# Kernel tuning notes

Measured on AMD Instinct MI355X. Metric: run time of the kernel, lower is better.

The kernel has to match this reference:

```python
import jax, jax.numpy as jnp
import numpy as np

ROPE_BASE = 10000.0

def _rope(x, positions):
    # x: (B, h, T, d); standard half-split rotary embedding with d_key = d
    d = x.shape[-1]
    inv_freq = 1.0 / (ROPE_BASE ** (jnp.arange(0, d // 2, dtype=jnp.float32) / (d // 2)))
    ang = positions.astype(jnp.float32)[:, None] * inv_freq[None, :]  # (T, d/2)
    cos, sin = jnp.cos(ang), jnp.sin(ang)
    x1, x2 = x[..., : d // 2], x[..., d // 2 :]
    return jnp.concatenate([x1 * cos - x2 * sin, x1 * sin + x2 * cos], axis=-1)


def setup_inputs() -> dict:
    key = jax.random.key(0)
    k1, k2, k3 = jax.random.split(key, 3)
    B, T, d, h = 2, 2048, 768, 8
    std = d ** -0.5
    x = jax.random.normal(k1, (B, T, d), dtype=jnp.float32)
    M = jax.random.normal(k2, (d, h * d), dtype=jnp.float32) * std
    V = jax.random.normal(k3, (d, h * d), dtype=jnp.float32) * std
    positions = jnp.arange(T, dtype=jnp.int32)
    return {"x": x, "M": M, "V": V, "positions": positions}


def reference(x, M, V, positions):
    B, T, d = x.shape
    h = M.shape[1] // d
    scale = 1.0 / jnp.sqrt(jnp.float32(d))
    # Q = RoPE(X @ M), K = RoPE(X) broadcast across heads, val = X @ V
    Q = (x @ M).reshape(B, T, h, d).transpose(0, 2, 1, 3)   # (B,h,T,d)
    val = (x @ V).reshape(B, T, h, d).transpose(0, 2, 1, 3)  # (B,h,T,d)
    K = jnp.broadcast_to(x[:, None, :, :], (B, h, T, d))     # (B,h,T,d)
    Q = _rope(Q, positions)
    K = _rope(K, positions)
    scores = jnp.einsum("bhqd,bhkd->bhqk", Q, K) * scale     # (B,h,T,T)
    causal = jnp.tril(jnp.ones((T, T), dtype=bool))          # True = keep
    scores = jnp.where(causal[None, None], scores, -jnp.inf)
    attn = jax.nn.softmax(scores, axis=-1)
    out = jnp.einsum("bhqk,bhkd->bhqd", attn, val)
    return out.sum(axis=1)  # sum over heads -> (B,T,d)
```

## Files before the change

kernel.cpp:

```cpp
#include <hip/hip_runtime.h>
#include <hip/hip_bf16.h>

typedef __bf16 bf16x8 __attribute__((ext_vector_type(8)));
typedef float f32x4 __attribute__((ext_vector_type(4)));
typedef float f32x16 __attribute__((ext_vector_type(16)));

#define SCALE 0.03608439182435161f
#define NEGINF (-1e30f)

static __device__ __forceinline__ ushort f2bf(float f) {
    union { float f; unsigned u; } v; v.f = f;
    unsigned r = (v.u + 0x7fff + ((v.u >> 16) & 1)) >> 16;
    return (ushort)r;
}
static __device__ __forceinline__ float bf2f(ushort u) {
    union { unsigned u; float f; } v; v.u = ((unsigned)u) << 16;
    return v.f;
}

static __device__ __forceinline__ void gload16(const void* g, void* lds) {
    __builtin_amdgcn_global_load_lds((const __attribute__((address_space(1))) void*)g,
                                     (__attribute__((address_space(3))) void*)lds, 16, 0, 0);
}

#define PHASEB do { asm volatile("s_waitcnt vmcnt(0) lgkmcnt(0)" ::: "memory"); \
                    __builtin_amdgcn_s_barrier(); \
                    asm volatile("" ::: "memory"); } while (0)
#define BARL do { asm volatile("s_waitcnt lgkmcnt(0)" ::: "memory"); \
                  __builtin_amdgcn_s_barrier(); \
                  asm volatile("" ::: "memory"); } while (0)

__global__ void k_convx(const float* __restrict__ x, ushort* __restrict__ xb, int n4) {
    int i = blockIdx.x * blockDim.x + threadIdx.x;
    if (i >= n4) return;
    float4 v = ((const float4*)x)[i];
    ushort4 o; o.x = f2bf(v.x); o.y = f2bf(v.y); o.z = f2bf(v.z); o.w = f2bf(v.w);
    ((ushort4*)xb)[i] = o;
}

__global__ void k_tconv(const float* __restrict__ in, ushort* __restrict__ out, int R, int C) {
    __shared__ float ts[32][33];
    int r0 = blockIdx.x * 32, c0 = blockIdx.y * 32;
    int lr = threadIdx.x >> 5, lc = threadIdx.x & 31;
#pragma unroll
    for (int i = 0; i < 4; i++) ts[lr + i * 8][lc] = in[(r0 + lr + i * 8) * C + c0 + lc];
    __syncthreads();
#pragma unroll
    for (int i = 0; i < 4; i++) out[(c0 + lr + i * 8) * R + r0 + lc] = f2bf(ts[lc][lr + i * 8]);
}

template <int EPI>
__global__ __launch_bounds__(256) void k_gemm(const ushort* __restrict__ A,
                                              const ushort* __restrict__ Bt,
                                              ushort* __restrict__ out) {
    __shared__ ushort As[128 * 32];
    __shared__ ushort Bs[128 * 32];
    const int m0 = blockIdx.x * 128, n0 = blockIdx.y * 128;
    const int tid = threadIdx.x, lane = tid & 63, wid = tid >> 6;
    const int wm = (wid >> 1) * 64, wn = (wid & 1) * 64;
    const int l15 = lane & 15, l4 = lane >> 4;
    const int srow = tid >> 2, scol = (tid & 3) * 8;
    f32x4 acc[4][4] = {};

    for (int kt = 0; kt < 768; kt += 32) {
        gload16(&A[(size_t)(m0 + srow) * 768 + kt + scol],       (char*)As + wid * 1024);
        gload16(&A[(size_t)(m0 + 64 + srow) * 768 + kt + scol],  (char*)As + 4096 + wid * 1024);
        gload16(&Bt[(size_t)(n0 + srow) * 768 + kt + scol],      (char*)Bs + wid * 1024);
        gload16(&Bt[(size_t)(n0 + 64 + srow) * 768 + kt + scol], (char*)Bs + 4096 + wid * 1024);
        PHASEB;
        bf16x8 af[4], bfr[4];
#pragma unroll
        for (int m = 0; m < 4; m++)
            af[m] = *(const bf16x8*)&As[(wm + m * 16 + l15) * 32 + l4 * 8];
#pragma unroll
        for (int n = 0; n < 4; n++)
            bfr[n] = *(const bf16x8*)&Bs[(wn + n * 16 + l15) * 32 + l4 * 8];
#pragma unroll
        for (int m = 0; m < 4; m++)
#pragma unroll
            for (int n = 0; n < 4; n++)
                acc[m][n] = __builtin_amdgcn_mfma_f32_16x16x32_bf16(af[m], bfr[n], acc[m][n], 0, 0, 0);
        BARL;
    }

#pragma unroll
    for (int m = 0; m < 4; m++) {
#pragma unroll
        for (int n = 0; n < 4; n++) {
#pragma unroll
            for (int r = 0; r < 4; r++) {
                int row = m0 + wm + m * 16 + (lane >> 4) * 4 + r;
                int col = n0 + wn + n * 16 + (lane & 15);
                float v = acc[m][n][r];
                int idx;
                if (EPI == 0) {
                    int b = row >> 11, t = row & 2047;
                    int hh = col / 768, dd = col - hh * 768;
                    idx = ((b * 8 + hh) * 2048 + t) * 768 + dd;
                } else {
                    int hh = row / 768, dd = row - hh * 768;
                    int b = col >> 11, t = col & 2047;
                    idx = ((b * 8 + hh) * 768 + dd) * 2048 + t;
                }
                out[idx] = f2bf(v);
            }
        }
    }
}

__global__ void k_ropek(const float* __restrict__ x, ushort* __restrict__ Kr,
                        const int* __restrict__ pos, int nrows) {
    int i = blockIdx.x * blockDim.x + threadIdx.x;
    int row = i / 96, j4 = (i % 96) * 4;
    if (row >= nrows) return;
    float p = (float)pos[row & 2047];
    float4 x1 = *(const float4*)&x[row * 768 + j4];
    float4 x2 = *(const float4*)&x[row * 768 + 384 + j4];
    ushort4 o1, o2;
    float a1[4] = {x1.x, x1.y, x1.z, x1.w};
    float a2[4] = {x2.x, x2.y, x2.z, x2.w};
#pragma unroll
    for (int k = 0; k < 4; k++) {
        float inv = exp2f(-(float)(j4 + k) * (13.287712379549449f / 384.0f));
        float ang = p * inv;
        float s, c; sincosf(ang, &s, &c);
        ((ushort*)&o1)[k] = f2bf(a1[k] * c - a2[k] * s);
        ((ushort*)&o2)[k] = f2bf(a1[k] * s + a2[k] * c);
    }
    *(ushort4*)&Kr[row * 768 + j4] = o1;
    *(ushort4*)&Kr[row * 768 + 384 + j4] = o2;
}

__global__ __launch_bounds__(512, 2) void k_attn(const ushort* Qr, const ushort* __restrict__ Kr,
                                                 const ushort* __restrict__ valT,
                                                 const int* __restrict__ pos, ushort* Oh) {
    __shared__ alignas(128) char Qs[98304];
    __shared__ alignas(128) char pool[65536];

    const int p = blockIdx.x, hh = blockIdx.y, b = blockIdx.z;
    const int bh = b * 8 + hh;
    const int tid = threadIdx.x, lane = tid & 63, wid = tid >> 6;
    const int g = wid & 3, qh = wid >> 2;
    const int l31 = lane & 31, hi = lane >> 5;
    const int hi16 = hi << 4;

    const int row0 = tid >> 4, col16 = tid & 15;
    const int swz = (col16 << 4) ^ ((row0 & 15) << 4);

    const int arow = g * 32 + l31;
    const int qrow = qh * 32 + l31;
    const int asw = (arow & 15) << 4;
    const int qsw = (qrow & 15) << 4;

    char* Pb = pool + 32768;
    float2* stats = (float2*)(pool + 49152);

    const char* Kb0 = (const char*)Kr + ((size_t)(b * 2048 + row0)) * 1536 + swz;
    const char* Vb0 = (const char*)valT + ((size_t)(bh * 768 + row0)) * 4096 + swz;

    for (int ti = 0; ti < 2; ti++) {
        const int qt = ti ? (31 - p) : p;
        const int q0 = qt * 64;
        const int nkb = (qt + 2) >> 1;
        const int qg = q0 + qrow;

        const char* qsrc = (const char*)Qr + ((size_t)(bh * 2048 + q0 + row0)) * 1536 + swz;
#pragma unroll
        for (int r = 0; r < 12; r++)
            gload16(qsrc + (r >> 1) * 256 + (size_t)(r & 1) * 49152,
                    Qs + (r >> 1) * 16384 + (r & 1) * 8192 + wid * 1024);
#pragma unroll
        for (int r = 0; r < 4; r++)
            gload16(Kb0 + (size_t)r * 49152, pool + r * 8192 + wid * 1024);

        PHASEB;

        {
            const int rr = tid >> 3;
            const int gb0 = (tid & 7) * 16;
            const int rsw = (rr & 15) << 4;
            const float pf = (float)pos[q0 + rr];
#pragma unroll
            for (int c = 0; c < 3; c++) {
#pragma unroll
                for (int h2 = 0; h2 < 2; h2++) {
                    int gb = gb0 + h2 * 128;
                    char* p1 = Qs + c * 16384 + rr * 256 + (gb ^ rsw);
                    char* p2 = Qs + (c + 3) * 16384 + rr * 256 + (gb ^ rsw);
                    uint4 u1 = *(uint4*)p1, u2 = *(uint4*)p2;
                    uint4 o1, o2;
                    ushort* a1 = (ushort*)&u1; ushort* a2 = (ushort*)&u2;
                    ushort* b1 = (ushort*)&o1; ushort* b2 = (ushort*)&o2;
#pragma unroll
                    for (int k = 0; k < 8; k++) {
                        float dv = (float)(c * 128 + (gb >> 1) + k);
                        float inv = exp2f(-dv * (13.287712379549449f / 384.0f));
                        float ang = pf * inv;
                        float sn, cs; __sincosf(ang, &sn, &cs);
                        float x1 = bf2f(a1[k]), x2 = bf2f(a2[k]);
                        b1[k] = f2bf((x1 * cs - x2 * sn) * SCALE);
                        b2[k] = f2bf((x1 * sn + x2 * cs) * SCALE);
                    }
                    *(uint4*)p1 = o1; *(uint4*)p2 = o2;
                }
            }
        }
        BARL;

        float m_r = NEGINF, l_r = 0.f;
        f32x16 oacc[6] = {};

        for (int kb = 0; kb < nkb; kb++) {
            const char* kc = Kb0 + (size_t)kb * 196608;
            const char* vc = Vb0 + (size_t)kb * 256;
            const bool nx = (kb + 1 < nkb);
            const bool nm = (kb * 128 + 127 > q0);

            f32x16 sacc = {};
#pragma unroll
            for (int c = 0; c < 6; c++) {
                PHASEB;
                if (c < 5) {
#pragma unroll
                    for (int r = 0; r < 4; r++)
                        gload16(kc + (c + 1) * 256 + (size_t)r * 49152,
                                pool + ((c + 1) & 1) * 32768 + r * 8192 + wid * 1024);
                } else {
#pragma unroll
                    for (int r = 0; r < 4; r++)
                        gload16(vc + (size_t)r * 131072, pool + r * 8192 + wid * 1024);
                }
                const char* kbuf = pool + (c & 1) * 32768;
                const char* qcb = Qs + c * 16384;
                __builtin_amdgcn_s_setprio(1);
#pragma unroll
                for (int s = 0; s < 8; s++) {
                    bf16x8 a = *(const bf16x8*)(kbuf + arow * 256 + ((s * 32 + hi16) ^ asw));
                    bf16x8 bq = *(const bf16x8*)(qcb + qrow * 256 + ((s * 32 + hi16) ^ qsw));
                    sacc = __builtin_amdgcn_mfma_f32_32x32x16_bf16(a, bq, sacc, 0, 0, 0);
                }
                __builtin_amdgcn_s_setprio(0);
            }

            BARL;

            const int kbase_ = kb * 128 + g * 32 + 4 * hi;
            float mloc = NEGINF, sloc = 0.f;
            if (nm) {
#pragma unroll
                for (int r = 0; r < 16; r++) {
                    int kg = kbase_ + (r & 3) + 8 * (r >> 2);
                    if (kg <= qg) mloc = fmaxf(mloc, sacc[r]);
                }
                mloc = fmaxf(mloc, __shfl_xor(mloc, 32));
#pragma unroll
                for (int r = 0; r < 16; r++) {
                    int kg = kbase_ + (r & 3) + 8 * (r >> 2);
                    sloc += (kg <= qg) ? __expf(sacc[r] - mloc) : 0.f;
                }
            } else {
#pragma unroll
                for (int r = 0; r < 16; r++) mloc = fmaxf(mloc, sacc[r]);
                mloc = fmaxf(mloc, __shfl_xor(mloc, 32));
#pragma unroll
                for (int r = 0; r < 16; r++) sloc += __expf(sacc[r] - mloc);
            }
            sloc += __shfl_xor(sloc, 32);
            if (hi == 0) stats[qrow * 4 + g] = make_float2(mloc, sloc);
            BARL;

            float4 sa = *(const float4*)(stats + qrow * 4);
            float4 sb = *(const float4*)(stats + qrow * 4 + 2);
            float m_new = fmaxf(fmaxf(fmaxf(sa.x, sa.z), fmaxf(sb.x, sb.z)), m_r);
            float rv = __expf(m_r - m_new);
            float lad = sa.y * __expf(sa.x - m_new) + sa.w * __expf(sa.z - m_new)
                      + sb.y * __expf(sb.x - m_new) + sb.w * __expf(sb.z - m_new);
            l_r = l_r * rv + lad; m_r = m_new;
            uint w[8];
            if (nm) {
#pragma unroll
                for (int j = 0; j < 8; j++) {
                    int kg0 = kbase_ + ((2 * j) & 3) + 8 * ((2 * j) >> 2);
                    int kg1 = kbase_ + ((2 * j + 1) & 3) + 8 * ((2 * j + 1) >> 2);
                    float e0 = (kg0 > qg) ? 0.f : __expf(sacc[2 * j] - m_new);
                    float e1 = (kg1 > qg) ? 0.f : __expf(sacc[2 * j + 1] - m_new);
                    w[j] = (uint)f2bf(e0) | ((uint)f2bf(e1) << 16);
                }
            } else {
#pragma unroll
                for (int j = 0; j < 8; j++) {
                    float e0 = __expf(sacc[2 * j] - m_new);
                    float e1 = __expf(sacc[2 * j + 1] - m_new);
                    w[j] = (uint)f2bf(e0) | ((uint)f2bf(e1) << 16);
                }
            }
#pragma unroll
            for (int j = 0; j < 4; j++) {
                uint2 pw; pw.x = w[2 * j]; pw.y = w[2 * j + 1];
                *(uint2*)(Pb + qrow * 256 + ((g * 64 + j * 16 + hi * 8) ^ qsw)) = pw;
            }
            BARL;

            float rs[16];
#pragma unroll
            for (int r = 0; r < 16; r++)
                rs[r] = __shfl(rv, (r & 3) + 8 * (r >> 2) + 4 * hi);
#pragma unroll
            for (int c = 0; c < 6; c++)
#pragma unroll
                for (int r = 0; r < 16; r++) oacc[c][r] *= rs[r];
            bf16x8 pa[8];
#pragma unroll
            for (int s = 0; s < 8; s++)
                pa[s] = *(const bf16x8*)(Pb + qrow * 256 + ((s * 32 + hi16) ^ qsw));

#pragma unroll
            for (int c = 0; c < 6; c++) {
                PHASEB;
                if (c < 5) {
#pragma unroll
                    for (int r = 0; r < 4; r++)
                        gload16(vc + (size_t)(c + 1) * 524288 + (size_t)r * 131072,
                                pool + ((c + 1) & 1) * 32768 + r * 8192 + wid * 1024);
                } else if (nx) {
#pragma unroll
                    for (int r = 0; r < 4; r++)
                        gload16(kc + 196608 + (size_t)r * 49152, pool + r * 8192 + wid * 1024);
                }
                const char* vbuf = pool + (c & 1) * 32768;
                __builtin_amdgcn_s_setprio(1);
#pragma unroll
                for (int s = 0; s < 8; s++) {
                    bf16x8 bv = *(const bf16x8*)(vbuf + arow * 256 + ((s * 32 + hi16) ^ asw));
                    oacc[c] = __builtin_amdgcn_mfma_f32_32x32x16_bf16(pa[s], bv, oacc[c], 0, 0, 0);
                }
                __builtin_amdgcn_s_setprio(0);
            }
        }

        float inv16[16];
#pragma unroll
        for (int r = 0; r < 16; r++)
            inv16[r] = 1.0f / __shfl(l_r, (r & 3) + 8 * (r >> 2) + 4 * hi);
        ushort* obase = Oh + ((size_t)(bh * 2048 + q0 + qh * 32)) * 768;
#pragma unroll
        for (int c = 0; c < 6; c++) {
            int dd = c * 128 + g * 32 + l31;
#pragma unroll
            for (int r = 0; r < 16; r++) {
                int rq = (r & 3) + 8 * (r >> 2) + 4 * hi;
                obase[(size_t)rq * 768 + dd] = f2bf(oacc[c][r] * inv16[r]);
            }
        }
    }
}

__global__ void k_reduce(const ushort* __restrict__ Oh, float* __restrict__ out) {
    int i = blockIdx.x * blockDim.x + threadIdx.x;
    if (i >= 786432) return;
    size_t base = (size_t)i * 4;
    int b = (base >= 1572864) ? 1 : 0;
    size_t rem = base - (size_t)b * 1572864;
    const ushort* src = Oh + (size_t)b * 8 * 1572864 + rem;
    float4 acc = {0.f, 0.f, 0.f, 0.f};
#pragma unroll
    for (int h = 0; h < 8; h++) {
        ushort4 v = *(const ushort4*)(src + (size_t)h * 1572864);
        acc.x += bf2f(v.x); acc.y += bf2f(v.y); acc.z += bf2f(v.z); acc.w += bf2f(v.w);
    }
    *(float4*)&out[base] = acc;
}

extern "C" void kernel_launch(void* const* d_in, const int* in_sizes, int n_in,
                              void* d_out, int out_size, void* d_ws, size_t ws_size,
                              hipStream_t stream) {
    const float* x = (const float*)d_in[0];
    const float* M = (const float*)d_in[1];
    const float* V = (const float*)d_in[2];
    const int* pos = (const int*)d_in[3];
    float* out = (float*)d_out;
    char* ws = (char*)d_ws;

    ushort* xb   = (ushort*)(ws);
    ushort* Mt   = (ushort*)(ws + 6291456);
    ushort* Vt   = (ushort*)(ws + 15728640);
    ushort* Qr   = (ushort*)(ws + 25165824);
    ushort* valT = (ushort*)(ws + 75497472);
    ushort* Kr   = (ushort*)(ws + 125829120);

    k_convx<<<3072, 256, 0, stream>>>(x, xb, 786432);
    k_tconv<<<dim3(24, 192), 256, 0, stream>>>(M, Mt, 768, 6144);
    k_tconv<<<dim3(24, 192), 256, 0, stream>>>(V, Vt, 768, 6144);
    k_gemm<0><<<dim3(32, 48), 256, 0, stream>>>(xb, Mt, Qr);
    k_gemm<1><<<dim3(48, 32), 256, 0, stream>>>(Vt, xb, valT);
    k_ropek<<<1536, 256, 0, stream>>>(x, Kr, pos, 4096);
    k_attn<<<dim3(16, 8, 2), 512, 0, stream>>>(Qr, Kr, valT, pos, Qr );
    k_reduce<<<3072, 256, 0, stream>>>(Qr, out);
}
```

Baseline: 354.4 us.

## Fuse Q RoPE and scaling into projection GEMM epilogue using precomputed sincos table

```diff
diff --git a/kernel.cpp b/kernel.cpp
--- a/kernel.cpp
+++ b/kernel.cpp
@@ -30,6 +30,16 @@
                   __builtin_amdgcn_s_barrier(); \
                   asm volatile("" ::: "memory"); } while (0)
 
+__global__ void k_tab(const int* __restrict__ pos, float2* __restrict__ tab) {
+    int i = blockIdx.x * blockDim.x + threadIdx.x;
+    if (i >= 786432) return;
+    int t = i / 384, u = i - t * 384;
+    float inv = exp2f(-(float)u * (13.287712379549449f / 384.0f));
+    float ang = (float)pos[t] * inv;
+    float s, c; sincosf(ang, &s, &c);
+    tab[i] = make_float2(c * SCALE, s * SCALE);
+}
+
 __global__ void k_convx(const float* __restrict__ x, ushort* __restrict__ xb, int n4) {
     int i = blockIdx.x * blockDim.x + threadIdx.x;
     if (i >= n4) return;
@@ -38,6 +48,7 @@
     ((ushort4*)xb)[i] = o;
 }
 
+template <int PERM>
 __global__ void k_tconv(const float* __restrict__ in, ushort* __restrict__ out, int R, int C) {
     __shared__ float ts[32][33];
     int r0 = blockIdx.x * 32, c0 = blockIdx.y * 32;
@@ -46,12 +57,20 @@
     for (int i = 0; i < 4; i++) ts[lr + i * 8][lc] = in[(r0 + lr + i * 8) * C + c0 + lc];
     __syncthreads();
 #pragma unroll
-    for (int i = 0; i < 4; i++) out[(c0 + lr + i * 8) * R + r0 + lc] = f2bf(ts[lc][lr + i * 8]);
+    for (int i = 0; i < 4; i++) {
+        int j = c0 + lr + i * 8;
+        if (PERM) {
+            int hh = j / 768, dd = j - hh * 768;
+            j = hh * 768 + ((dd < 384) ? (dd << 1) : (((dd - 384) << 1) | 1));
+        }
+        out[j * R + r0 + lc] = f2bf(ts[lc][lr + i * 8]);
+    }
 }
 
 template <int EPI>
 __global__ __launch_bounds__(256) void k_gemm(const ushort* __restrict__ A,
                                               const ushort* __restrict__ Bt,
+                                              const float2* __restrict__ tab,
                                               ushort* __restrict__ out) {
     __shared__ ushort As[128 * 32];
     __shared__ ushort Bs[128 * 32];
@@ -89,20 +108,24 @@
         for (int n = 0; n < 4; n++) {
 #pragma unroll
             for (int r = 0; r < 4; r++) {
-                int row = m0 + wm + m * 16 + (lane >> 4) * 4 + r;
-                int col = n0 + wn + n * 16 + (lane & 15);
+                int row = m0 + wm + m * 16 + l4 * 4 + r;
+                int col = n0 + wn + n * 16 + l15;
                 float v = acc[m][n][r];
-                int idx;
                 if (EPI == 0) {
+                    float vp = __shfl_xor(v, 1);
                     int b = row >> 11, t = row & 2047;
-                    int hh = col / 768, dd = col - hh * 768;
-                    idx = ((b * 8 + hh) * 2048 + t) * 768 + dd;
+                    int hh = col / 768, cp = col - hh * 768;
+                    int u = cp >> 1;
+                    float2 cs = tab[t * 384 + u];
+                    float ov = (cp & 1) ? (v * cs.x + vp * cs.y)
+                                        : (v * cs.x - vp * cs.y);
+                    int dd = (cp & 1) ? u + 384 : u;
+                    out[((b * 8 + hh) * 2048 + t) * 768 + dd] = f2bf(ov);
                 } else {
                     int hh = row / 768, dd = row - hh * 768;
                     int b = col >> 11, t = col & 2047;
-                    idx = ((b * 8 + hh) * 768 + dd) * 2048 + t;
-                }
-                out[idx] = f2bf(v);
+                    out[((b * 8 + hh) * 768 + dd) * 2048 + t] = f2bf(v);
+                }
             }
         }
     }
@@ -132,8 +155,7 @@
 }
 
 __global__ __launch_bounds__(512, 2) void k_attn(const ushort* Qr, const ushort* __restrict__ Kr,
-                                                 const ushort* __restrict__ valT,
-                                                 const int* __restrict__ pos, ushort* Oh) {
+                                                 const ushort* __restrict__ valT, ushort* Oh) {
     __shared__ alignas(128) char Qs[98304];
     __shared__ alignas(128) char pool[65536];
 
@@ -172,40 +194,6 @@
 #pragma unroll
         for (int r = 0; r < 4; r++)
             gload16(Kb0 + (size_t)r * 49152, pool + r * 8192 + wid * 1024);
-
-        PHASEB;
-
-        {
-            const int rr = tid >> 3;
-            const int gb0 = (tid & 7) * 16;
-            const int rsw = (rr & 15) << 4;
-            const float pf = (float)pos[q0 + rr];
-#pragma unroll
-            for (int c = 0; c < 3; c++) {
-#pragma unroll
-                for (int h2 = 0; h2 < 2; h2++) {
-                    int gb = gb0 + h2 * 128;
-                    char* p1 = Qs + c * 16384 + rr * 256 + (gb ^ rsw);
-                    char* p2 = Qs + (c + 3) * 16384 + rr * 256 + (gb ^ rsw);
-                    uint4 u1 = *(uint4*)p1, u2 = *(uint4*)p2;
-                    uint4 o1, o2;
-                    ushort* a1 = (ushort*)&u1; ushort* a2 = (ushort*)&u2;
-                    ushort* b1 = (ushort*)&o1; ushort* b2 = (ushort*)&o2;
-#pragma unroll
-                    for (int k = 0; k < 8; k++) {
-                        float dv = (float)(c * 128 + (gb >> 1) + k);
-                        float inv = exp2f(-dv * (13.287712379549449f / 384.0f));
-                        float ang = pf * inv;
-                        float sn, cs; __sincosf(ang, &sn, &cs);
-                        float x1 = bf2f(a1[k]), x2 = bf2f(a2[k]);
-                        b1[k] = f2bf((x1 * cs - x2 * sn) * SCALE);
-                        b2[k] = f2bf((x1 * sn + x2 * cs) * SCALE);
-                    }
-                    *(uint4*)p1 = o1; *(uint4*)p2 = o2;
-                }
-            }
-        }
-        BARL;
 
         float m_r = NEGINF, l_r = 0.f;
         f32x16 oacc[6] = {};
@@ -387,13 +375,15 @@
     ushort* Qr   = (ushort*)(ws + 25165824);
     ushort* valT = (ushort*)(ws + 75497472);
     ushort* Kr   = (ushort*)(ws + 125829120);
-
+    float2* tab  = (float2*)(ws + 125829120);
+
+    k_tab<<<3072, 256, 0, stream>>>(pos, tab);
     k_convx<<<3072, 256, 0, stream>>>(x, xb, 786432);
-    k_tconv<<<dim3(24, 192), 256, 0, stream>>>(M, Mt, 768, 6144);
-    k_tconv<<<dim3(24, 192), 256, 0, stream>>>(V, Vt, 768, 6144);
-    k_gemm<0><<<dim3(32, 48), 256, 0, stream>>>(xb, Mt, Qr);
-    k_gemm<1><<<dim3(48, 32), 256, 0, stream>>>(Vt, xb, valT);
+    k_tconv<1><<<dim3(24, 192), 256, 0, stream>>>(M, Mt, 768, 6144);
+    k_tconv<0><<<dim3(24, 192), 256, 0, stream>>>(V, Vt, 768, 6144);
+    k_gemm<0><<<dim3(32, 48), 256, 0, stream>>>(xb, Mt, tab, Qr);
+    k_gemm<1><<<dim3(48, 32), 256, 0, stream>>>(Vt, xb, nullptr, valT);
     k_ropek<<<1536, 256, 0, stream>>>(x, Kr, pos, 4096);
-    k_attn<<<dim3(16, 8, 2), 512, 0, stream>>>(Qr, Kr, valT, pos, Qr );
+    k_attn<<<dim3(16, 8, 2), 512, 0, stream>>>(Qr, Kr, valT, Qr );
     k_reduce<<<3072, 256, 0, stream>>>(Qr, out);
 }
```

Measured after the change: 364.5 us. 2.9% more time.
